# Kernel tuning notes

Measured on AMD Instinct MI355X. Metric: run time of the kernel, lower is better.

## Reference

```python
import jax, jax.numpy as jnp
import numpy as np

D_MODEL = 256
NUM_HEADS = 8
HEAD_DIM = D_MODEL // NUM_HEADS
B, L = 2, 2048


def setup_inputs() -> dict:
    key = jax.random.key(0)
    ks = jax.random.split(key, 16)
    s = 0.02
    return {
        "query": jax.random.normal(ks[0], (B, L, D_MODEL), jnp.float32),
        "key": jax.random.normal(ks[1], (B, L, D_MODEL), jnp.float32),
        "value": jax.random.normal(ks[2], (B, L, D_MODEL), jnp.float32),
        "struct_bias": jax.random.normal(ks[3], (B, NUM_HEADS, L, L), jnp.float32),
        "attn_mask": jax.random.normal(ks[4], (B, NUM_HEADS, L, L), jnp.float32),
        "Wq": jax.random.normal(ks[5], (D_MODEL, D_MODEL), jnp.float32) * s,
        "bq": jnp.zeros((D_MODEL,), jnp.float32),
        "Wk": jax.random.normal(ks[6], (D_MODEL, D_MODEL), jnp.float32) * s,
        "bk": jnp.zeros((D_MODEL,), jnp.float32),
        "Wv": jax.random.normal(ks[7], (D_MODEL, D_MODEL), jnp.float32) * s,
        "bv": jnp.zeros((D_MODEL,), jnp.float32),
        "Wo": jax.random.normal(ks[8], (D_MODEL, D_MODEL), jnp.float32) * s,
        "bo": jnp.zeros((D_MODEL,), jnp.float32),
    }


def reference(query, key, value, struct_bias, attn_mask,
              Wq, bq, Wk, bk, Wv, bv, Wo, bo):
    b, t, _ = query.shape
    # projections (torch Linear: x @ W.T + b)
    q = query @ Wq.T + bq
    k = key @ Wk.T + bk
    v = value @ Wv.T + bv
    # [B, H, L, Dh]
    q = q.reshape(b, t, NUM_HEADS, HEAD_DIM).transpose(0, 2, 1, 3)
    k = k.reshape(b, t, NUM_HEADS, HEAD_DIM).transpose(0, 2, 1, 3)
    v = v.reshape(b, t, NUM_HEADS, HEAD_DIM).transpose(0, 2, 1, 3)
    scale = 1.0 / np.sqrt(HEAD_DIM).astype(np.float32)
    scores = jnp.einsum("bhqd,bhkd->bhqk", q, k) * scale
    scores = scores + struct_bias + attn_mask
    attn_weights = jax.nn.softmax(scores, axis=-1)
    context = jnp.einsum("bhqk,bhkd->bhqd", attn_weights, v)
    context = context.transpose(0, 2, 1, 3).reshape(b, t, D_MODEL)
    output = context @ Wo.T + bo
    return (output, attn_weights)
```

## Files before the change

### kernel.cpp

```cpp
#include <hip/hip_runtime.h>

typedef __bf16 bf16x8 __attribute__((ext_vector_type(8)));
typedef __bf16 bf16x4 __attribute__((ext_vector_type(4)));
typedef short  s16x8  __attribute__((ext_vector_type(8)));
typedef float  f32x4  __attribute__((ext_vector_type(4)));

#define MFMA16(a,b,c) __builtin_amdgcn_mfma_f32_16x16x32_bf16((a),(b),(c),0,0,0)

static constexpr float SCALE = 0.17677669529663687f;

__device__ __forceinline__ unsigned short f2b(float f){
  __bf16 h = (__bf16)f;
  return __builtin_bit_cast(unsigned short, h);
}
__device__ __forceinline__ bf16x8 ldfrag(const unsigned short* p){
  s16x8 v = *(const s16x8*)p;
  return __builtin_bit_cast(bf16x8, v);
}
__device__ __forceinline__ bf16x8 cvt8(const float* p){
  f32x4 a = *(const f32x4*)p;
  f32x4 b = *(const f32x4*)(p+4);
  bf16x8 r;
  r[0]=(__bf16)a[0]; r[1]=(__bf16)a[1]; r[2]=(__bf16)a[2]; r[3]=(__bf16)a[3];
  r[4]=(__bf16)b[0]; r[5]=(__bf16)b[1]; r[6]=(__bf16)b[2]; r[7]=(__bf16)b[3];
  return r;
}

__device__ __forceinline__ void bar_lgkm(){
  asm volatile("s_waitcnt lgkmcnt(0)" ::: "memory");
  __builtin_amdgcn_s_barrier();
  __builtin_amdgcn_sched_barrier(0);
}

__global__ __launch_bounds__(256) void proj_kernel(
    const float* __restrict__ xq, const float* __restrict__ xk, const float* __restrict__ xv,
    const float* __restrict__ Wq, const float* __restrict__ bq,
    const float* __restrict__ Wk, const float* __restrict__ bk,
    const float* __restrict__ Wv, const float* __restrict__ bv,
    unsigned short* __restrict__ qo, unsigned short* __restrict__ ko,
    unsigned short* __restrict__ vT)
{
  const int z = blockIdx.z;
  const float* x    = (z==0) ? xq : (z==1 ? xk : xv);
  const float* W    = (z==0) ? Wq : (z==1 ? Wk : Wv);
  const float* bias = (z==0) ? bq : (z==1 ? bk : bv);
  const int tid = threadIdx.x, w = tid>>6, l = tid&63;
  const int m0 = blockIdx.x*16;
  const int n0 = blockIdx.y*64 + w*16;
  const int ra = l&15, ko8 = (l>>4)*8;

  __shared__ unsigned short xs[16*264];
  #pragma unroll
  for(int i=0;i<4;++i){
    int chunk = tid + i*256;
    int row = chunk>>6, c4 = (chunk&63)*4;
    f32x4 v = *(const f32x4*)(x + (m0+row)*256 + c4);
    ushort4 u; u.x=f2b(v[0]); u.y=f2b(v[1]); u.z=f2b(v[2]); u.w=f2b(v[3]);
    *(ushort4*)(&xs[row*264 + c4]) = u;
  }
  __syncthreads();

  f32x4 acc = {0.f,0.f,0.f,0.f};
  #pragma unroll
  for(int kk=0;kk<8;++kk){
    int kb = kk*32 + ko8;
    bf16x8 a   = ldfrag(&xs[ra*264 + kb]);
    bf16x8 bfr = cvt8(W + (n0+ra)*256 + kb);
    acc = MFMA16(a, bfr, acc);
  }
  const int col = l&15;
  const int n = n0 + col;
  const float bval = bias[n];

  __shared__ float vt[4][16][17];
  if(z < 2){
    unsigned short* out = (z==0) ? qo : ko;
    #pragma unroll
    for(int r=0;r<4;++r){
      int R = (l>>4)*4 + r, m = m0 + R;
      float val = acc[r] + bval;
      if(z==0) val *= SCALE;
      int bidx = m>>11, ls = m&2047, hh = n>>5, dh = n&31;
      out[(((long)(bidx*8+hh))*2048 + ls)*32 + dh] = f2b(val);
    }
  } else {
    #pragma unroll
    for(int r=0;r<4;++r){
      int R = (l>>4)*4 + r;
      vt[w][R][col] = acc[r] + bval;
    }
    __syncthreads();
    int bidx = m0>>11, hh = n0>>5, dh0 = n0&31, bh = bidx*8 + hh;
    int lsc = m0 & 2047;
    int dloc = l>>2, kloc = (l&3)*4;
    ushort4 pk;
    pk.x = f2b(vt[w][kloc+0][dloc]);
    pk.y = f2b(vt[w][kloc+1][dloc]);
    pk.z = f2b(vt[w][kloc+2][dloc]);
    pk.w = f2b(vt[w][kloc+3][dloc]);
    *reinterpret_cast<ushort4*>(vT + ((long)(bh*32 + dh0 + dloc))*2048 + lsc + kloc) = pk;
  }
}

__global__ __launch_bounds__(1024) void attn_kernel(
    const unsigned short* __restrict__ qbf, const unsigned short* __restrict__ kbf,
    const unsigned short* __restrict__ vT,
    const float* __restrict__ sbias, const float* __restrict__ amask,
    float* __restrict__ Pout, float* __restrict__ ctx)
{
  __shared__ unsigned short sS[16*2048];
  __shared__ float linv[16];

  const int tid = threadIdx.x, w = tid>>6, l = tid&63;
  const int q0 = blockIdx.x*16;
  const int h = blockIdx.y, b = blockIdx.z;
  const int bh = b*8 + h;
  const long qkbase = (long)bh*2048*32;
  const long vbase  = (long)bh*32*2048;
  const long bmbase = ((long)bh*2048 + q0)*2048;
  const long rowbase = bmbase + (long)w*2048;
  const int ws = w*128;
  const int col = l&15, ko8 = (l>>4)*8, rg = (l>>4)*4;
  const int swq = (col&7)<<3;
  const int sww = (w&7)<<3;
  const f32x4 zero = {0.f,0.f,0.f,0.f};

  bf16x8 aq = ldfrag(qbf + qkbase + (long)(q0+col)*32 + ko8);
  #pragma unroll
  for(int t=0;t<8;++t){
    int key0 = ws + t*16;
    bf16x8 kf = ldfrag(kbf + qkbase + (long)(key0+col)*32 + ko8);
    f32x4 acc = MFMA16(kf, aq, zero);
    bf16x4 s4; s4[0]=(__bf16)acc[0]; s4[1]=(__bf16)acc[1];
    s4[2]=(__bf16)acc[2]; s4[3]=(__bf16)acc[3];
    *(bf16x4*)(&sS[col*2048 + ((key0+rg) ^ swq)]) = s4;
  }

  f32x4 s[8];
  #pragma unroll
  for(int k=0;k<8;++k){
    long c = rowbase + k*256 + l*4;
    f32x4 b4 = __builtin_nontemporal_load((const f32x4*)(sbias + c));
    f32x4 m4 = __builtin_nontemporal_load((const f32x4*)(amask + c));
    s[k] = b4 + m4;
  }
  bar_lgkm();

  float m = -1e30f;
  #pragma unroll
  for(int k=0;k<8;++k){
    int c = k*256 + l*4;
    bf16x4 r4 = *(const bf16x4*)(&sS[w*2048 + (c ^ sww)]);
    s[k][0]+=(float)r4[0]; s[k][1]+=(float)r4[1];
    s[k][2]+=(float)r4[2]; s[k][3]+=(float)r4[3];
    m = fmaxf(m, fmaxf(fmaxf(s[k][0],s[k][1]), fmaxf(s[k][2],s[k][3])));
  }
  #pragma unroll
  for(int d=1;d<64;d<<=1) m = fmaxf(m, __shfl_xor(m, d));
  float sum = 0.f;
  #pragma unroll
  for(int k=0;k<8;++k){
    s[k][0]=__expf(s[k][0]-m); s[k][1]=__expf(s[k][1]-m);
    s[k][2]=__expf(s[k][2]-m); s[k][3]=__expf(s[k][3]-m);
    sum += (s[k][0]+s[k][1]) + (s[k][2]+s[k][3]);
  }
  #pragma unroll
  for(int d=1;d<64;d<<=1) sum += __shfl_xor(sum, d);
  const float li = 1.0f/sum;
  if(l==0) linv[w] = li;

  #pragma unroll
  for(int k=0;k<8;++k){
    int c = k*256 + l*4;
    f32x4 p; p[0]=s[k][0]*li; p[1]=s[k][1]*li; p[2]=s[k][2]*li; p[3]=s[k][3]*li;
    __builtin_nontemporal_store(p, (f32x4*)(Pout + rowbase + c));
    bf16x4 e4; e4[0]=(__bf16)s[k][0]; e4[1]=(__bf16)s[k][1];
    e4[2]=(__bf16)s[k][2]; e4[3]=(__bf16)s[k][3];
    *(bf16x4*)(&sS[w*2048 + (c ^ sww)]) = e4;
  }
  bar_lgkm();

  f32x4 acc0 = zero, acc1 = zero;
  #pragma unroll
  for(int c4=0;c4<4;++c4){
    int kb = ws + c4*32 + ko8;
    bf16x8 pa = ldfrag(&sS[col*2048 + (kb ^ swq)]);
    bf16x8 v0 = ldfrag(vT + vbase + (long)col*2048 + kb);
    bf16x8 v1 = ldfrag(vT + vbase + (long)(16+col)*2048 + kb);
    acc0 = MFMA16(pa, v0, acc0);
    acc1 = MFMA16(pa, v1, acc1);
  }
  bar_lgkm();

  float* sF = (float*)sS;
  #pragma unroll
  for(int r=0;r<4;++r){
    int R = rg + r;
    sF[w*512 + R*32 + col]      = acc0[r];
    sF[w*512 + R*32 + 16 + col] = acc1[r];
  }
  bar_lgkm();

  if(tid < 512){
    int row = tid>>5, dh = tid&31;
    float ssum = 0.f;
    #pragma unroll
    for(int w2=0; w2<16; ++w2) ssum += sF[w2*512 + row*32 + dh];
    ctx[((long)b*2048 + q0 + row)*256 + h*32 + dh] = ssum * linv[row];
  }
}

__global__ __launch_bounds__(256) void oproj_kernel(
    float* __restrict__ out0, const float* __restrict__ Wo, const float* __restrict__ bo)
{
  __shared__ unsigned short lct[8*264];
  const int tid = threadIdx.x, w = tid>>6, l = tid&63;
  const int m0 = blockIdx.x*8;
  #pragma unroll
  for(int i=0;i<2;++i){
    int chunk = tid + i*256;
    int row = chunk>>6, c4 = (chunk&63)*4;
    f32x4 v = *(const f32x4*)(out0 + (m0+row)*256 + c4);
    ushort4 u; u.x=f2b(v[0]); u.y=f2b(v[1]); u.z=f2b(v[2]); u.w=f2b(v[3]);
    *(ushort4*)(&lct[row*264 + c4]) = u;
  }
  __syncthreads();
  const int col = l&15, ko8 = (l>>4)*8, rg = (l>>4)*4;
  const int arow = col&7;
  #pragma unroll
  for(int nt=0;nt<4;++nt){
    int n0 = w*64 + nt*16;
    f32x4 acc = {0.f,0.f,0.f,0.f};
    #pragma unroll
    for(int kk=0;kk<8;++kk){
      int kb = kk*32 + ko8;
      bf16x8 a   = ldfrag(&lct[arow*264 + kb]);
      bf16x8 bfr = cvt8(Wo + (n0+col)*256 + kb);
      acc = MFMA16(a, bfr, acc);
    }
    float bv = bo[n0+col];
    if(rg < 8){
      #pragma unroll
      for(int r=0;r<4;++r){
        out0[(m0+rg+r)*256 + n0+col] = acc[r] + bv;
      }
    }
  }
}

extern "C" void kernel_launch(void* const* d_in, const int* in_sizes, int n_in,
                              void* d_out, int out_size, void* d_ws, size_t ws_size,
                              hipStream_t stream)
{
  const float* query = (const float*)d_in[0];
  const float* key   = (const float*)d_in[1];
  const float* value = (const float*)d_in[2];
  const float* sbias = (const float*)d_in[3];
  const float* amask = (const float*)d_in[4];
  const float* Wq = (const float*)d_in[5];
  const float* bq = (const float*)d_in[6];
  const float* Wk = (const float*)d_in[7];
  const float* bk = (const float*)d_in[8];
  const float* Wv = (const float*)d_in[9];
  const float* bv = (const float*)d_in[10];
  const float* Wo = (const float*)d_in[11];
  const float* bo = (const float*)d_in[12];

  float* out0 = (float*)d_out;
  float* Pout = out0 + (size_t)2*2048*256;

  unsigned short* qbf = (unsigned short*)d_ws;
  unsigned short* kbf = qbf + (size_t)2*8*2048*32;
  unsigned short* vTb = kbf + (size_t)2*8*2048*32;

  proj_kernel<<<dim3(256,4,3), 256, 0, stream>>>(query,key,value,Wq,bq,Wk,bk,Wv,bv,qbf,kbf,vTb);
  attn_kernel<<<dim3(128,8,2), 1024, 0, stream>>>(qbf,kbf,vTb,sbias,amask,Pout,out0);
  oproj_kernel<<<dim3(512), 256, 0, stream>>>(out0,Wo,bo);
}
```

Baseline: 206.5 us.

## Process two 16-row query tiles per attention block with overlapped bias loads

Each attention block now handles 32 query rows as two 16-row tiles. K fragments are held in registers and reused for both tiles. The second tile's bias and mask loads are issued before the first tile's PV matmul, and its QK^T runs before the first tile's context reduction, so memory traffic overlaps compute. A separate 32KB shared buffer for context partials raises LDS use per block, and the grid is halved, which may lower occupancy and parallelism.

```diff
diff --git a/kernel.cpp b/kernel.cpp
--- a/kernel.cpp
+++ b/kernel.cpp
@@ -109,48 +109,50 @@
     float* __restrict__ Pout, float* __restrict__ ctx)
 {
   __shared__ unsigned short sS[16*2048];
-  __shared__ float linv[16];
+  __shared__ float cbuf[16*512];
+  __shared__ float linv0[16], linv1[16];
 
   const int tid = threadIdx.x, w = tid>>6, l = tid&63;
-  const int q0 = blockIdx.x*16;
+  const int q0 = blockIdx.x*32;
   const int h = blockIdx.y, b = blockIdx.z;
   const int bh = b*8 + h;
   const long qkbase = (long)bh*2048*32;
   const long vbase  = (long)bh*32*2048;
-  const long bmbase = ((long)bh*2048 + q0)*2048;
-  const long rowbase = bmbase + (long)w*2048;
   const int ws = w*128;
   const int col = l&15, ko8 = (l>>4)*8, rg = (l>>4)*4;
   const int swq = (col&7)<<3;
   const int sww = (w&7)<<3;
   const f32x4 zero = {0.f,0.f,0.f,0.f};
-
-  bf16x8 aq = ldfrag(qbf + qkbase + (long)(q0+col)*32 + ko8);
+  const long row0 = ((long)bh*2048 + q0 + w)*2048;
+  const long row1 = row0 + 16*2048;
+
+  bf16x8 kf[8];
+  #pragma unroll
+  for(int t=0;t<8;++t)
+    kf[t] = ldfrag(kbf + qkbase + (long)(ws + t*16 + col)*32 + ko8);
+  bf16x8 aq0 = ldfrag(qbf + qkbase + (long)(q0+col)*32 + ko8);
+  bf16x8 aq1 = ldfrag(qbf + qkbase + (long)(q0+16+col)*32 + ko8);
+
   #pragma unroll
   for(int t=0;t<8;++t){
-    int key0 = ws + t*16;
-    bf16x8 kf = ldfrag(kbf + qkbase + (long)(key0+col)*32 + ko8);
-    f32x4 acc = MFMA16(kf, aq, zero);
+    f32x4 acc = MFMA16(kf[t], aq0, zero);
     bf16x4 s4; s4[0]=(__bf16)acc[0]; s4[1]=(__bf16)acc[1];
     s4[2]=(__bf16)acc[2]; s4[3]=(__bf16)acc[3];
-    *(bf16x4*)(&sS[col*2048 + ((key0+rg) ^ swq)]) = s4;
-  }
-
+    *(bf16x4*)(&sS[col*2048 + ((ws + t*16 + rg) ^ swq)]) = s4;
+  }
   f32x4 s[8];
   #pragma unroll
   for(int k=0;k<8;++k){
-    long c = rowbase + k*256 + l*4;
-    f32x4 b4 = __builtin_nontemporal_load((const f32x4*)(sbias + c));
-    f32x4 m4 = __builtin_nontemporal_load((const f32x4*)(amask + c));
-    s[k] = b4 + m4;
+    long c = row0 + k*256 + l*4;
+    s[k] = __builtin_nontemporal_load((const f32x4*)(sbias + c))
+         + __builtin_nontemporal_load((const f32x4*)(amask + c));
   }
   bar_lgkm();
 
   float m = -1e30f;
   #pragma unroll
   for(int k=0;k<8;++k){
-    int c = k*256 + l*4;
-    bf16x4 r4 = *(const bf16x4*)(&sS[w*2048 + (c ^ sww)]);
+    bf16x4 r4 = *(const bf16x4*)(&sS[w*2048 + ((k*256 + l*4) ^ sww)]);
     s[k][0]+=(float)r4[0]; s[k][1]+=(float)r4[1];
     s[k][2]+=(float)r4[2]; s[k][3]+=(float)r4[3];
     m = fmaxf(m, fmaxf(fmaxf(s[k][0],s[k][1]), fmaxf(s[k][2],s[k][3])));
@@ -166,47 +168,118 @@
   }
   #pragma unroll
   for(int d=1;d<64;d<<=1) sum += __shfl_xor(sum, d);
-  const float li = 1.0f/sum;
-  if(l==0) linv[w] = li;
+  float li = 1.0f/sum;
+  if(l==0) linv0[w] = li;
 
   #pragma unroll
   for(int k=0;k<8;++k){
     int c = k*256 + l*4;
     f32x4 p; p[0]=s[k][0]*li; p[1]=s[k][1]*li; p[2]=s[k][2]*li; p[3]=s[k][3]*li;
-    __builtin_nontemporal_store(p, (f32x4*)(Pout + rowbase + c));
+    __builtin_nontemporal_store(p, (f32x4*)(Pout + row0 + c));
     bf16x4 e4; e4[0]=(__bf16)s[k][0]; e4[1]=(__bf16)s[k][1];
     e4[2]=(__bf16)s[k][2]; e4[3]=(__bf16)s[k][3];
     *(bf16x4*)(&sS[w*2048 + (c ^ sww)]) = e4;
   }
-  bar_lgkm();
-
-  f32x4 acc0 = zero, acc1 = zero;
+  #pragma unroll
+  for(int k=0;k<8;++k){
+    long c = row1 + k*256 + l*4;
+    s[k] = __builtin_nontemporal_load((const f32x4*)(sbias + c))
+         + __builtin_nontemporal_load((const f32x4*)(amask + c));
+  }
+  bar_lgkm();
+
+  f32x4 a0 = zero, a1 = zero;
   #pragma unroll
   for(int c4=0;c4<4;++c4){
     int kb = ws + c4*32 + ko8;
     bf16x8 pa = ldfrag(&sS[col*2048 + (kb ^ swq)]);
     bf16x8 v0 = ldfrag(vT + vbase + (long)col*2048 + kb);
     bf16x8 v1 = ldfrag(vT + vbase + (long)(16+col)*2048 + kb);
-    acc0 = MFMA16(pa, v0, acc0);
-    acc1 = MFMA16(pa, v1, acc1);
-  }
-  bar_lgkm();
-
-  float* sF = (float*)sS;
+    a0 = MFMA16(pa, v0, a0);
+    a1 = MFMA16(pa, v1, a1);
+  }
+  bar_lgkm();
+
   #pragma unroll
   for(int r=0;r<4;++r){
     int R = rg + r;
-    sF[w*512 + R*32 + col]      = acc0[r];
-    sF[w*512 + R*32 + 16 + col] = acc1[r];
+    cbuf[w*512 + R*32 + col]      = a0[r];
+    cbuf[w*512 + R*32 + 16 + col] = a1[r];
+  }
+  #pragma unroll
+  for(int t=0;t<8;++t){
+    f32x4 acc = MFMA16(kf[t], aq1, zero);
+    bf16x4 s4; s4[0]=(__bf16)acc[0]; s4[1]=(__bf16)acc[1];
+    s4[2]=(__bf16)acc[2]; s4[3]=(__bf16)acc[3];
+    *(bf16x4*)(&sS[col*2048 + ((ws + t*16 + rg) ^ swq)]) = s4;
   }
   bar_lgkm();
 
   if(tid < 512){
     int row = tid>>5, dh = tid&31;
-    float ssum = 0.f;
-    #pragma unroll
-    for(int w2=0; w2<16; ++w2) ssum += sF[w2*512 + row*32 + dh];
-    ctx[((long)b*2048 + q0 + row)*256 + h*32 + dh] = ssum * linv[row];
+    float ss = 0.f;
+    #pragma unroll
+    for(int w2=0; w2<16; ++w2) ss += cbuf[w2*512 + row*32 + dh];
+    ctx[((long)b*2048 + q0 + row)*256 + h*32 + dh] = ss * linv0[row];
+  }
+
+  m = -1e30f;
+  #pragma unroll
+  for(int k=0;k<8;++k){
+    bf16x4 r4 = *(const bf16x4*)(&sS[w*2048 + ((k*256 + l*4) ^ sww)]);
+    s[k][0]+=(float)r4[0]; s[k][1]+=(float)r4[1];
+    s[k][2]+=(float)r4[2]; s[k][3]+=(float)r4[3];
+    m = fmaxf(m, fmaxf(fmaxf(s[k][0],s[k][1]), fmaxf(s[k][2],s[k][3])));
+  }
+  #pragma unroll
+  for(int d=1;d<64;d<<=1) m = fmaxf(m, __shfl_xor(m, d));
+  sum = 0.f;
+  #pragma unroll
+  for(int k=0;k<8;++k){
+    s[k][0]=__expf(s[k][0]-m); s[k][1]=__expf(s[k][1]-m);
+    s[k][2]=__expf(s[k][2]-m); s[k][3]=__expf(s[k][3]-m);
+    sum += (s[k][0]+s[k][1]) + (s[k][2]+s[k][3]);
+  }
+  #pragma unroll
+  for(int d=1;d<64;d<<=1) sum += __shfl_xor(sum, d);
+  li = 1.0f/sum;
+  if(l==0) linv1[w] = li;
+
+  #pragma unroll
+  for(int k=0;k<8;++k){
+    int c = k*256 + l*4;
+    f32x4 p; p[0]=s[k][0]*li; p[1]=s[k][1]*li; p[2]=s[k][2]*li; p[3]=s[k][3]*li;
+    __builtin_nontemporal_store(p, (f32x4*)(Pout + row1 + c));
+    bf16x4 e4; e4[0]=(__bf16)s[k][0]; e4[1]=(__bf16)s[k][1];
+    e4[2]=(__bf16)s[k][2]; e4[3]=(__bf16)s[k][3];
+    *(bf16x4*)(&sS[w*2048 + (c ^ sww)]) = e4;
+  }
+  bar_lgkm();
+
+  a0 = zero; a1 = zero;
+  #pragma unroll
+  for(int c4=0;c4<4;++c4){
+    int kb = ws + c4*32 + ko8;
+    bf16x8 pa = ldfrag(&sS[col*2048 + (kb ^ swq)]);
+    bf16x8 v0 = ldfrag(vT + vbase + (long)col*2048 + kb);
+    bf16x8 v1 = ldfrag(vT + vbase + (long)(16+col)*2048 + kb);
+    a0 = MFMA16(pa, v0, a0);
+    a1 = MFMA16(pa, v1, a1);
+  }
+  #pragma unroll
+  for(int r=0;r<4;++r){
+    int R = rg + r;
+    cbuf[w*512 + R*32 + col]      = a0[r];
+    cbuf[w*512 + R*32 + 16 + col] = a1[r];
+  }
+  bar_lgkm();
+
+  if(tid < 512){
+    int row = tid>>5, dh = tid&31;
+    float ss = 0.f;
+    #pragma unroll
+    for(int w2=0; w2<16; ++w2) ss += cbuf[w2*512 + row*32 + dh];
+    ctx[((long)b*2048 + q0 + 16 + row)*256 + h*32 + dh] = ss * linv1[row];
   }
 }
 
@@ -274,6 +347,6 @@
   unsigned short* vTb = kbf + (size_t)2*8*2048*32;
 
   proj_kernel<<<dim3(256,4,3), 256, 0, stream>>>(query,key,value,Wq,bq,Wk,bk,Wv,bv,qbf,kbf,vTb);
-  attn_kernel<<<dim3(128,8,2), 1024, 0, stream>>>(qbf,kbf,vTb,sbias,amask,Pout,out0);
+  attn_kernel<<<dim3(64,8,2), 1024, 0, stream>>>(qbf,kbf,vTb,sbias,amask,Pout,out0);
   oproj_kernel<<<dim3(512), 256, 0, stream>>>(out0,Wo,bo);
 }
```

Result: slower. 262.8 us (+27.2%).
